# Kernel optimization log

Measured on AMD Instinct MI355X. Metric: run time of the kernel, lower is better.

The kernel has to match this reference:

```python
import jax, jax.numpy as jnp
import numpy as np

BS = 4          # batch size
SEQ = 128       # max_seqlen == batch_seq_len
LAYERS = 6      # transformer_block_count
HEADS = 32      # attn_head_count
HEAD_DIM = 128  # attn_head_dim
STRIDE = 16     # block_pos_stride
FEAT = HEADS * HEAD_DIM          # 4096
BLOCKS = SEQ // STRIDE           # 8 seq blocks per sequence
PAGES = 128                      # chosen page-table size
CACHE_LINES = 2                  # k and v
PAGE_STRIDE = LAYERS * CACHE_LINES  # 12 sub-blocks per page


def setup_inputs() -> dict:
    key = jax.random.key(0)
    k1, k2 = jax.random.split(key)
    seq_lens = jax.random.randint(k1, (BS,), 0, SEQ, dtype=jnp.int32)
    attn_block_ids = jnp.arange(BS * BLOCKS, dtype=jnp.int32).reshape(BS, BLOCKS)
    attn_page_slab = jax.random.normal(k2, (PAGES, LAYERS, CACHE_LINES, STRIDE, HEADS, HEAD_DIM), dtype=jnp.float32)
    return {"seq_lens": seq_lens, "attn_block_ids": attn_block_ids, "attn_page_slab": attn_page_slab}


def reference(seq_lens, attn_block_ids, attn_page_slab):
    # Flatten slab to sub-block granularity: [PAGES*LAYERS*2, STRIDE, HEADS, HEAD_DIM]
    slab = attn_page_slab.reshape(-1, STRIDE, HEADS, HEAD_DIM)
    ids = attn_block_ids.reshape(-1)  # [BS*BLOCKS]
    h = jnp.ones((BS, SEQ, FEAT), dtype=attn_page_slab.dtype)
    for layer in range(LAYERS):
        xk = 2.0 * h
        xv = 4.0 * h
        # computed page-table addresses (paged KV-cache scatter write)
        k_ids = ids * PAGE_STRIDE + layer * CACHE_LINES
        kb = xk.reshape(BS * BLOCKS, STRIDE, HEADS, HEAD_DIM)
        vb = xv.reshape(BS * BLOCKS, STRIDE, HEADS, HEAD_DIM)
        slab = slab.at[k_ids].set(kb)
        slab = slab.at[k_ids + 1].set(vb)
        # attention_output = x * xk * xv = 8*x^3 ; h = h + attention_output
        h = h + h * xk * xv
    return h, slab.reshape(attn_page_slab.shape)
```

## Files before the change

### kernel.cpp

```cpp
#include <hip/hip_runtime.h>

#define N_LAYERS    6
#define PAGE_STRIDE 12
#define N_SUBBLOCKS 1536
#define SUB_U4_LOG2 13
#define H_LANES     2097152
#define SLAB_LANES  100663296
#define H_U4        (H_LANES / 8)
#define SLAB_U4     (SLAB_LANES / 8)
#define TOTAL_U4    (H_U4 + SLAB_U4)
#define MAIN_BLOCKS (TOTAL_U4 / 1024)
#define TAB_WORDS   (N_SUBBLOCKS + 1)

typedef unsigned int ux4 __attribute__((ext_vector_type(4)));

__device__ __forceinline__ float opq(float x) {
    asm volatile("" : "+v"(x));
    return x;
}

__device__ __forceinline__ unsigned bf16_rne_clamped(float x) {
    unsigned b  = __float_as_uint(opq(x));
    unsigned hi = b >> 16, lo = b & 0xFFFFu;
    hi += (lo > 0x8000u) || ((lo == 0x8000u) && (hi & 1u));
    if ((hi & 0x7F80u) == 0x7F80u) hi = 0x7F7Fu;
    return hi;
}

__device__ __forceinline__ float h_layer(int n) {
    float h = opq(1.0f);
    for (int l = 0; l < n; ++l) {
        float xk = opq(__fmul_rn(2.0f, h));
        float xv = opq(__fmul_rn(4.0f, h));
        float t  = opq(__fmul_rn(h, xk));
        t        = opq(__fmul_rn(t, xv));
        h        = opq(__fadd_rn(h, t));
    }
    return h;
}

__global__ void build_table_kernel(const int* __restrict__ ids, int n_ids,
                                   unsigned* __restrict__ tab) {
    int sb = blockIdx.x * blockDim.x + threadIdx.x;
    if (sb >= TAB_WORDS) return;
    unsigned w;
    if (sb == N_SUBBLOCKS) {
        unsigned hb = bf16_rne_clamped(h_layer(N_LAYERS));
        w = (hb << 16) | hb;
    } else {
        int page = sb / PAGE_STRIDE;
        int sub  = sb - page * PAGE_STRIDE;
        bool hit = false;
        for (int j = 0; j < n_ids; ++j) hit |= (ids[j] == page);
        w = 0u;
        if (hit) {
            float m = (sub & 1) ? 4.0f : 2.0f;
            unsigned b = bf16_rne_clamped(__fmul_rn(m, h_layer(sub >> 1)));
            w = (b << 16) | b;
        }
    }
    tab[sb] = w;
}

__global__ __launch_bounds__(256) void stream_kernel(
        const ux4* __restrict__ in,
        ux4* __restrict__ out,
        const unsigned* __restrict__ tab) {
    const int base = blockIdx.x * 1024 + threadIdx.x;
    unsigned w[4];
    ux4 r[4];
#pragma unroll
    for (int k = 0; k < 4; ++k) {
        int g  = base + k * 256;
        int sb = (g < H_U4) ? N_SUBBLOCKS : ((g - H_U4) >> SUB_U4_LOG2);
        w[k] = tab[sb];
        if (w[k] == 0u) {
            r[k] = __builtin_nontemporal_load(&in[g - H_U4]);
        }
    }
#pragma unroll
    for (int k = 0; k < 4; ++k) {
        int g = base + k * 256;
        ux4 v;
        if (w[k] != 0u) {
            v = (ux4){w[k], w[k], w[k], w[k]};
        } else {
            v = r[k];
        }
        __builtin_nontemporal_store(v, &out[g]);
    }
}

extern "C" void kernel_launch(void* const* d_in, const int* in_sizes, int n_in,
                              void* d_out, int out_size, void* d_ws, size_t ws_size,
                              hipStream_t stream) {
    const int* ids = (const int*)d_in[1];
    int n_ids = in_sizes[1];

    unsigned* tab = (unsigned*)d_ws;

    build_table_kernel<<<(TAB_WORDS + 255) / 256, 256, 0, stream>>>(ids, n_ids, tab);

    stream_kernel<<<MAIN_BLOCKS, 256, 0, stream>>>(
        (const ux4*)d_in[2], (ux4*)d_out, tab);
}
```

Measured before the change: 69.76 us.

## Fuse table build into stream kernel and process one sub-block quarter per block

Removes the separate table-building kernel launch. Each block now computes its own fill word from the block ids, and the block size is sized so that every block falls inside a single sub-block. Each thread moves 8 vectors instead of 4, and a whole block branches uniformly between a constant fill and a copy. This saves one launch plus the per-element table lookups. The cost is that every block rescans the ids (32 entries) and recomputes the layer recurrence.

Measured after the change: 65.42 us. 1.07x faster.

```diff
diff --git a/kernel.cpp b/kernel.cpp
--- a/kernel.cpp
+++ b/kernel.cpp
@@ -1,16 +1,13 @@
 #include <hip/hip_runtime.h>
 
-#define N_LAYERS    6
-#define PAGE_STRIDE 12
-#define N_SUBBLOCKS 1536
-#define SUB_U4_LOG2 13
-#define H_LANES     2097152
-#define SLAB_LANES  100663296
-#define H_U4        (H_LANES / 8)
-#define SLAB_U4     (SLAB_LANES / 8)
-#define TOTAL_U4    (H_U4 + SLAB_U4)
-#define MAIN_BLOCKS (TOTAL_U4 / 1024)
-#define TAB_WORDS   (N_SUBBLOCKS + 1)
+#define N_LAYERS     6
+#define PAGE_STRIDE  12
+#define N_SUBBLOCKS  1536
+#define H_U4         262144
+#define TOTAL_U4     12845056
+#define U4_PER_BLOCK 2048
+#define MAIN_BLOCKS  (TOTAL_U4 / U4_PER_BLOCK)
+#define H_BLOCKS     (H_U4 / U4_PER_BLOCK)
 
 typedef unsigned int ux4 __attribute__((ext_vector_type(4)));
 
@@ -39,15 +36,18 @@
     return h;
 }
 
-__global__ void build_table_kernel(const int* __restrict__ ids, int n_ids,
-                                   unsigned* __restrict__ tab) {
-    int sb = blockIdx.x * blockDim.x + threadIdx.x;
-    if (sb >= TAB_WORDS) return;
+__global__ __launch_bounds__(256) void fused_stream_kernel(
+        const ux4* __restrict__ in,
+        ux4* __restrict__ out,
+        const int* __restrict__ ids, int n_ids) {
+    const int blk = blockIdx.x;
+
     unsigned w;
-    if (sb == N_SUBBLOCKS) {
+    if (blk < H_BLOCKS) {
         unsigned hb = bf16_rne_clamped(h_layer(N_LAYERS));
         w = (hb << 16) | hb;
     } else {
+        int sb   = (blk - H_BLOCKS) >> 2;
         int page = sb / PAGE_STRIDE;
         int sub  = sb - page * PAGE_STRIDE;
         bool hit = false;
@@ -59,35 +59,22 @@
             w = (b << 16) | b;
         }
     }
-    tab[sb] = w;
-}
 
-__global__ __launch_bounds__(256) void stream_kernel(
-        const ux4* __restrict__ in,
-        ux4* __restrict__ out,
-        const unsigned* __restrict__ tab) {
-    const int base = blockIdx.x * 1024 + threadIdx.x;
-    unsigned w[4];
-    ux4 r[4];
+    const int base = blk * U4_PER_BLOCK + threadIdx.x;
+    if (w != 0u) {
+        ux4 v = (ux4){w, w, w, w};
 #pragma unroll
-    for (int k = 0; k < 4; ++k) {
-        int g  = base + k * 256;
-        int sb = (g < H_U4) ? N_SUBBLOCKS : ((g - H_U4) >> SUB_U4_LOG2);
-        w[k] = tab[sb];
-        if (w[k] == 0u) {
-            r[k] = __builtin_nontemporal_load(&in[g - H_U4]);
-        }
-    }
+        for (int k = 0; k < 8; ++k)
+            __builtin_nontemporal_store(v, &out[base + k * 256]);
+    } else {
+        const ux4* src = in + (base - H_U4);
+        ux4 r[8];
 #pragma unroll
-    for (int k = 0; k < 4; ++k) {
-        int g = base + k * 256;
-        ux4 v;
-        if (w[k] != 0u) {
-            v = (ux4){w[k], w[k], w[k], w[k]};
-        } else {
-            v = r[k];
-        }
-        __builtin_nontemporal_store(v, &out[g]);
+        for (int k = 0; k < 8; ++k)
+            r[k] = __builtin_nontemporal_load(&src[k * 256]);
+#pragma unroll
+        for (int k = 0; k < 8; ++k)
+            __builtin_nontemporal_store(r[k], &out[base + k * 256]);
     }
 }
 
@@ -97,10 +84,6 @@
     const int* ids = (const int*)d_in[1];
     int n_ids = in_sizes[1];
 
-    unsigned* tab = (unsigned*)d_ws;
-
-    build_table_kernel<<<(TAB_WORDS + 255) / 256, 256, 0, stream>>>(ids, n_ids, tab);
-
-    stream_kernel<<<MAIN_BLOCKS, 256, 0, stream>>>(
-        (const ux4*)d_in[2], (ux4*)d_out, tab);
+    fused_stream_kernel<<<MAIN_BLOCKS, 256, 0, stream>>>(
+        (const ux4*)d_in[2], (ux4*)d_out, ids, n_ids);
 }
```
